# Optimization experiments

Measured on AMD Instinct MI355X. Metric: run time of the kernel, lower is better.

The kernel has to match this reference:

```python
import jax, jax.numpy as jnp
import numpy as np

D = 196; NCH = 64; H = 8; DH = 64; INNER = H * DH; MLP = 784; SEQ = 65


def _ln(x, g, b, eps=1e-5):
    m = x.mean(-1, keepdims=True)
    v = x.var(-1, keepdims=True)
    return (x - m) / jnp.sqrt(v + eps) * g + b


def setup_inputs() -> dict:
    key = jax.random.key(0)
    ks = jax.random.split(key, 12)
    f = jax.random.normal
    return dict(
        x=f(ks[0], (1, SEQ, D), dtype=jnp.float32),
        tokens=f(ks[1], (1, D), dtype=jnp.float32),
        x_pe=f(ks[2], (1, NCH, D), dtype=jnp.float32),
        conv_k=f(ks[3], (3, 3), dtype=jnp.float32) * 0.3,   # Conv2d(1,1,3) kernel
        bn_g=jnp.ones(()), bn_b=jnp.zeros(()), bn_rm=jnp.zeros(()), bn_rv=jnp.ones(()),
        fc_w1=f(ks[4], (NCH, 12)) * 0.1,
        fc_w2=f(ks[5], (12, NCH)) * 0.1,
        ln1_g=jnp.ones((D,)), ln1_b=jnp.zeros((D,)),
        ln2_g=jnp.ones((D,)), ln2_b=jnp.zeros((D,)),
        w_qkv=f(ks[6], (D, 3 * INNER)) * 0.05,
        w_out=f(ks[7], (INNER, D)) * 0.05, b_out=jnp.zeros((D,)),
        ff_w1=f(ks[8], (D, MLP)) * 0.05, ff_b1=jnp.zeros((MLP,)),
        ff_w2=f(ks[9], (MLP, D)) * 0.05, ff_b2=jnp.zeros((D,)),
    )


def reference(x, tokens, x_pe, conv_k, bn_g, bn_b, bn_rm, bn_rv,
              fc_w1, fc_w2, ln1_g, ln1_b, ln2_g, ln2_b,
              w_qkv, w_out, b_out, ff_w1, ff_b1, ff_w2, ff_b2):
    # --- per-channel Conv2d(1,1,3,p=1)+BN+ReLU, batched over all 64 rows ---
    # Each row is (1,1,1,196): height 1 with pad 1 means the top/bottom kernel
    # rows only touch zero padding, so only the middle kernel row contributes
    # -> equivalent to a 1D conv with kernel conv_k[1].
    rows = x_pe[0]                      # [64,196]
    km = conv_k[1]                      # [3]
    xp = jnp.pad(rows, ((0, 0), (1, 1)))
    conv = km[0] * xp[:, :D] + km[1] * xp[:, 1:D + 1] + km[2] * xp[:, 2:D + 2]
    bn = (conv - bn_rm) / jnp.sqrt(bn_rv + 1e-5) * bn_g + bn_b
    a = jax.nn.relu(bn)                 # [64,196]  (== x_AfterConv / a)

    # --- sort-based suppress/excitation channel gating ---
    b1 = a.mean(-1)                     # [64] adaptive avg pool
    val = jnp.sort(b1)
    idx = jnp.argsort(b1)
    middle = jnp.where((val.max() < 0) | (val.min() > 0),
                       jnp.int32(32), jnp.argmax(val > 0).astype(jnp.int32))
    rank = jnp.argsort(idx)             # rank of each channel in ascending order
    sup = rank < middle                 # channels in idx[:middle]
    l_s = middle.astype(b1.dtype)
    l_e = (NCH - middle).astype(b1.dtype)
    b2 = jnp.where(sup,
                   b1 - 1.0 / (1.0 + jnp.power(l_s, b1)),
                   b1 + 1.0 / (1.0 + jnp.power(l_e, -b1)))

    c = jax.nn.sigmoid(jax.nn.relu(b2 @ fc_w1) @ fc_w2)   # [64]
    x_att = a * c[:, None]                                  # [64,196]
    x_att = jnp.concatenate([x_att, tokens.reshape(1, D)], axis=0)[None]  # [1,65,196]

    # --- PreNorm attention ---
    h = _ln(x, ln1_g, ln1_b)
    qkv = h @ w_qkv
    q, k, v = jnp.split(qkv, 3, axis=-1)
    def heads(t):
        return t.reshape(1, SEQ, H, DH).transpose(0, 2, 1, 3)  # b h n d
    q, k, v = heads(q), heads(k), heads(v)
    attn = jax.nn.softmax(jnp.einsum('bhnd,bhmd->bhnm', q, k) * (DH ** -0.5), axis=-1)
    o = jnp.einsum('bhnm,bhmd->bhnd', attn, v).transpose(0, 2, 1, 3).reshape(1, SEQ, INNER)
    x = o @ w_out + b_out + x + x_att

    # --- PreNorm feed-forward ---
    h2 = _ln(x, ln2_g, ln2_b)
    x = (jax.nn.gelu(h2 @ ff_w1 + ff_b1, approximate=False) @ ff_w2 + ff_b2) + x
    return x
```

## Files before the change

kernel.cpp:

```cpp
#include <hip/hip_runtime.h>
#include <math.h>

#define D 196
#define NCH 64
#define NH 8
#define DHD 64
#define INNER 512
#define MLP 784
#define SEQ 65

__device__ __forceinline__ float bsum(float v, float* red) {
    for (int off = 32; off > 0; off >>= 1) v += __shfl_down(v, off, 64);
    int lane = threadIdx.x & 63, wid = threadIdx.x >> 6;
    if (lane == 0) red[wid] = v;
    __syncthreads();
    float s = red[0] + red[1] + red[2] + red[3];
    __syncthreads();
    return s;
}

__device__ __forceinline__ float bsum8(float v, float* red) {
    for (int off = 32; off > 0; off >>= 1) v += __shfl_down(v, off, 64);
    int lane = threadIdx.x & 63, wid = threadIdx.x >> 6;
    if (lane == 0) red[wid] = v;
    __syncthreads();
    float s = red[0] + red[1] + red[2] + red[3] + red[4] + red[5] + red[6] + red[7];
    __syncthreads();
    return s;
}

__global__ void __launch_bounds__(256) k1(const float* __restrict__ x_pe,
        const float* __restrict__ conv_k, const float* __restrict__ bn_g,
        const float* __restrict__ bn_b, const float* __restrict__ bn_rm,
        const float* __restrict__ bn_rv, const float* __restrict__ x,
        const float* __restrict__ ln1_g, const float* __restrict__ ln1_b,
        const float* __restrict__ w_qkv,
        float* __restrict__ a, float* __restrict__ b1, float* __restrict__ qkv) {
    __shared__ float red[4];
    __shared__ float h[D];
    __shared__ float ps[512];
    int b = blockIdx.x, t = threadIdx.x;
    if (b < NCH) {
        const float* row = x_pe + b * D;
        float val = 0.f;
        if (t < D) {
            float km0 = conv_k[3], km1 = conv_k[4], km2 = conv_k[5];
            float inv = rsqrtf(bn_rv[0] + 1e-5f);
            float l = (t > 0) ? row[t - 1] : 0.f;
            float m = row[t];
            float r = (t < D - 1) ? row[t + 1] : 0.f;
            float conv = km0 * l + km1 * m + km2 * r;
            float bn = (conv - bn_rm[0]) * inv * bn_g[0] + bn_b[0];
            val = fmaxf(bn, 0.f);
            a[b * D + t] = val;
        }
        float tot = bsum(val, red);
        if (t == 0) b1[b] = tot * (1.f / (float)D);
    } else {
        int qb = b - NCH;
        int n = qb / 12, cg = qb % 12;
        const float* row = x + n * D;
        float v = (t < D) ? row[t] : 0.f;
        float mean = bsum(v, red) * (1.f / (float)D);
        float d = (t < D) ? (v - mean) : 0.f;
        float var = bsum(d * d, red) * (1.f / (float)D);
        float rinv = rsqrtf(var + 1e-5f);
        if (t < D) h[t] = d * rinv * ln1_g[t] + ln1_b[t];
        __syncthreads();
        int qq = t >> 6, lt = t & 63;
        int c0 = cg * 128 + lt * 2;
        const float* wp = w_qkv + (qq * 49) * 1536 + c0;
        const float* hp = h + qq * 49;
        float a0 = 0.f, a1 = 0.f;
#pragma unroll
        for (int i = 0; i < 49; i++) {
            float2 w2 = *(const float2*)(wp + i * 1536);
            float hv = hp[i];
            a0 += hv * w2.x;
            a1 += hv * w2.y;
        }
        ps[qq * 128 + lt * 2] = a0;
        ps[qq * 128 + lt * 2 + 1] = a1;
        __syncthreads();
        if (t < 64) {
            float s0 = ps[t * 2] + ps[128 + t * 2] + ps[256 + t * 2] + ps[384 + t * 2];
            float s1 = ps[t * 2 + 1] + ps[129 + t * 2] + ps[257 + t * 2] + ps[385 + t * 2];
            float2 o2 = make_float2(s0, s1);
            *(float2*)(qkv + n * 1536 + cg * 128 + t * 2) = o2;
        }
    }
}

__global__ void __launch_bounds__(512) k2(const float* __restrict__ b1,
        const float* __restrict__ fc_w1, const float* __restrict__ fc_w2,
        const float* __restrict__ qkv, const float* __restrict__ w_out,
        const float* __restrict__ b_out, const float* __restrict__ x,
        const float* __restrict__ a, const float* __restrict__ tokens,
        const float* __restrict__ ln2_g, const float* __restrict__ ln2_b,
        const float* __restrict__ ff_b2,
        float* __restrict__ h2g, float* __restrict__ out) {
    __shared__ float red[8];
    __shared__ float sq[512];
    __shared__ float pp[8 * 80];
    __shared__ float so[512];
    __shared__ float ps[784];
    __shared__ float x2row[D];
    __shared__ float sb1[NCH];
    __shared__ float sb2[NCH];
    __shared__ float hid[12];
    __shared__ float cgate;

    int n = blockIdx.x, t = threadIdx.x;

    sq[t] = qkv[n * 1536 + t];
    if (t < NCH) sb1[t] = b1[t];
    __syncthreads();
    if (t < NCH) {
        float v = sb1[t];
        float mx = -1e30f, mn = 1e30f;
        int cle = 0, rank = 0;
        for (int j = 0; j < NCH; j++) {
            float w = sb1[j];
            mx = fmaxf(mx, w);
            mn = fminf(mn, w);
            if (w <= 0.f) cle++;
            if (w < v || (w == v && j < t)) rank++;
        }
        int middle;
        if (mx < 0.f || mn > 0.f) middle = 32;
        else if (mx <= 0.f) middle = 0;
        else middle = cle;
        float b2;
        if (rank < middle) {
            float ls = (float)middle;
            b2 = v - 1.f / (1.f + powf(ls, v));
        } else {
            float le = (float)(NCH - middle);
            b2 = v + 1.f / (1.f + powf(le, -v));
        }
        sb2[t] = b2;
    }
    __syncthreads();
    if (t < 12) {
        float s = 0.f;
        for (int j = 0; j < NCH; j++) s += sb2[j] * fc_w1[j * 12 + t];
        hid[t] = fmaxf(s, 0.f);
    }
    __syncthreads();
    if (t == 0 && n < NCH) {
        float s = 0.f;
        for (int k = 0; k < 12; k++) s += hid[k] * fc_w2[k * NCH + n];
        cgate = 1.f / (1.f + expf(-s));
    }
    __syncthreads();

    const float scale = 0.125f;
    int w = t >> 6, L = t & 63;
    const float4* kr = (const float4*)(qkv + L * 1536 + INNER + w * DHD);
    const float4* q4 = (const float4*)(sq + w * DHD);
    float s = 0.f;
#pragma unroll
    for (int i = 0; i < 16; i++) {
        float4 kv = kr[i];
        float4 qv = q4[i];
        s += qv.x * kv.x + qv.y * kv.y + qv.z * kv.z + qv.w * kv.w;
    }
    float sL = s * scale;
    float t64 = sq[w * DHD + L] * qkv[64 * 1536 + INNER + w * DHD + L];
#pragma unroll
    for (int off = 1; off < 64; off <<= 1) t64 += __shfl_xor(t64, off, 64);
    float s64 = t64 * scale;
    float mx = sL;
#pragma unroll
    for (int off = 1; off < 64; off <<= 1) mx = fmaxf(mx, __shfl_xor(mx, off, 64));
    mx = fmaxf(mx, s64);
    float e = expf(sL - mx);
    float e64 = expf(s64 - mx);
    float esum = e;
#pragma unroll
    for (int off = 1; off < 64; off <<= 1) esum += __shfl_xor(esum, off, 64);
    esum += e64;
    float rs = 1.f / esum;
    pp[w * 80 + L] = e;
    if (L == 0) pp[w * 80 + 64] = e64;
    __syncthreads();
    float acc = 0.f;
#pragma unroll 13
    for (int m = 0; m < SEQ; m++)
        acc += pp[w * 80 + m] * qkv[m * 1536 + 2 * INNER + w * DHD + L];
    so[w * DHD + L] = acc * rs;
    __syncthreads();

    if (t < 392) {
        int qq = t / 98, p = t - qq * 98;
        const float* wp = w_out + (qq * 128) * D + 2 * p;
        const float* op = so + qq * 128;
        float a0 = 0.f, a1 = 0.f;
#pragma unroll 16
        for (int i = 0; i < 128; i++) {
            float2 w2 = *(const float2*)(wp + i * D);
            float ov = op[i];
            a0 += ov * w2.x;
            a1 += ov * w2.y;
        }
        ps[qq * 196 + 2 * p] = a0;
        ps[qq * 196 + 2 * p + 1] = a1;
    }
    __syncthreads();
    if (t < 98) {
        float s0 = ps[2 * t] + ps[196 + 2 * t] + ps[392 + 2 * t] + ps[588 + 2 * t];
        float s1 = ps[2 * t + 1] + ps[197 + 2 * t] + ps[393 + 2 * t] + ps[589 + 2 * t];
        float2 xr = *(const float2*)(x + n * D + 2 * t);
        float2 br = *(const float2*)(b_out + 2 * t);
        x2row[2 * t] = s0 + xr.x + br.x;
        x2row[2 * t + 1] = s1 + xr.y + br.y;
    }
    __syncthreads();

    if (t < D) {
        float att = (n < NCH) ? a[n * D + t] * cgate : tokens[t];
        float xv = x2row[t] + att;
        x2row[t] = xv;
        out[n * D + t] = xv + ff_b2[t];
    }
    __syncthreads();

    float v = (t < D) ? x2row[t] : 0.f;
    float mean = bsum8(v, red) * (1.f / (float)D);
    float d = (t < D) ? (v - mean) : 0.f;
    float var = bsum8(d * d, red) * (1.f / (float)D);
    float rinv = rsqrtf(var + 1e-5f);
    if (t < D) h2g[n * D + t] = d * rinv * ln2_g[t] + ln2_b[t];
}

__global__ void __launch_bounds__(256) k3(const float* __restrict__ h2g,
        const float* __restrict__ ff_w1, const float* __restrict__ ff_b1,
        const float* __restrict__ ff_w2, float* __restrict__ out) {
    __shared__ float h2s[D];
    __shared__ float st[98];
    __shared__ float ps[392];
    int n = blockIdx.x, cg = blockIdx.y, t = threadIdx.x;
    if (t < D) h2s[t] = h2g[n * D + t];
    __syncthreads();
    if (t < D) {
        int qq = t / 49, p = t - qq * 49;
        int c0 = cg * 98 + 2 * p;
        const float* wp = ff_w1 + (qq * 49) * MLP + c0;
        const float* hp = h2s + qq * 49;
        float a0 = 0.f, a1 = 0.f;
#pragma unroll
        for (int i = 0; i < 49; i++) {
            float2 w2 = *(const float2*)(wp + i * MLP);
            float hv = hp[i];
            a0 += hv * w2.x;
            a1 += hv * w2.y;
        }
        if (qq == 0) { a0 += ff_b1[c0]; a1 += ff_b1[c0 + 1]; }
        ps[qq * 98 + 2 * p] = a0;
        ps[qq * 98 + 2 * p + 1] = a1;
    }
    __syncthreads();
    if (t < 49) {
        float s0 = ps[2 * t] + ps[98 + 2 * t] + ps[196 + 2 * t] + ps[294 + 2 * t];
        float s1 = ps[2 * t + 1] + ps[99 + 2 * t] + ps[197 + 2 * t] + ps[295 + 2 * t];
        st[2 * t] = 0.5f * s0 * (1.f + erff(s0 * 0.70710678118f));
        st[2 * t + 1] = 0.5f * s1 * (1.f + erff(s1 * 0.70710678118f));
    }
    __syncthreads();
    if (t < D) {
        int hh = t / 98, p = t - hh * 98;
        const float* wp = ff_w2 + (cg * 98 + hh * 49) * D + 2 * p;
        const float* sp = st + hh * 49;
        float a0 = 0.f, a1 = 0.f;
#pragma unroll
        for (int i = 0; i < 49; i++) {
            float2 w2 = *(const float2*)(wp + i * D);
            float sv = sp[i];
            a0 += sv * w2.x;
            a1 += sv * w2.y;
        }
        ps[hh * 196 + 2 * p] = a0;
        ps[hh * 196 + 2 * p + 1] = a1;
    }
    __syncthreads();
    if (t < 98) {
        float s0 = ps[2 * t] + ps[196 + 2 * t];
        float s1 = ps[2 * t + 1] + ps[197 + 2 * t];
        atomicAdd(&out[n * D + 2 * t], s0);
        atomicAdd(&out[n * D + 2 * t + 1], s1);
    }
}

extern "C" void kernel_launch(void* const* d_in, const int* in_sizes, int n_in,
                              void* d_out, int out_size, void* d_ws, size_t ws_size,
                              hipStream_t stream) {
    const float* x      = (const float*)d_in[0];
    const float* tokens = (const float*)d_in[1];
    const float* x_pe   = (const float*)d_in[2];
    const float* conv_k = (const float*)d_in[3];
    const float* bn_g   = (const float*)d_in[4];
    const float* bn_b   = (const float*)d_in[5];
    const float* bn_rm  = (const float*)d_in[6];
    const float* bn_rv  = (const float*)d_in[7];
    const float* fc_w1  = (const float*)d_in[8];
    const float* fc_w2  = (const float*)d_in[9];
    const float* ln1_g  = (const float*)d_in[10];
    const float* ln1_b  = (const float*)d_in[11];
    const float* ln2_g  = (const float*)d_in[12];
    const float* ln2_b  = (const float*)d_in[13];
    const float* w_qkv  = (const float*)d_in[14];
    const float* w_out  = (const float*)d_in[15];
    const float* b_out  = (const float*)d_in[16];
    const float* ff_w1  = (const float*)d_in[17];
    const float* ff_b1  = (const float*)d_in[18];
    const float* ff_w2  = (const float*)d_in[19];
    const float* ff_b2  = (const float*)d_in[20];
    float* out = (float*)d_out;

    float* ws = (float*)d_ws;
    float* a    = ws;
    float* b1   = ws + 12544;
    float* qkv  = ws + 12608;
    float* h2g  = ws + 112448;

    k1<<<844, 256, 0, stream>>>(x_pe, conv_k, bn_g, bn_b, bn_rm, bn_rv,
                                x, ln1_g, ln1_b, w_qkv, a, b1, qkv);
    k2<<<SEQ, 512, 0, stream>>>(b1, fc_w1, fc_w2, qkv, w_out, b_out, x,
                                a, tokens, ln2_g, ln2_b, ff_b2, h2g, out);
    k3<<<dim3(SEQ, 8), 256, 0, stream>>>(h2g, ff_w1, ff_b1, ff_w2, out);
}
```

Before: 137.4 us.

## Split attention kernel across head groups and move LayerNorm2 into FFN kernel

The attention/output-projection kernel now runs two 256-thread blocks per token, each handling four heads. Partial output-projection results are combined with atomics into a workspace row that k1 zeroes beforehand. LayerNorm2 and the residual/bias add move into the feed-forward kernel, and each of its column-group blocks recomputes the row norm. This raises parallelism in the latency-bound middle stage and drops the h2g round trip. The costs are redundant LN work in k3, extra atomics, and reliance on single-wavefront ordering for some shared-memory reads that no longer have a barrier.

```diff
diff --git a/kernel.cpp b/kernel.cpp
--- a/kernel.cpp
+++ b/kernel.cpp
@@ -19,28 +19,21 @@
     return s;
 }
 
-__device__ __forceinline__ float bsum8(float v, float* red) {
-    for (int off = 32; off > 0; off >>= 1) v += __shfl_down(v, off, 64);
-    int lane = threadIdx.x & 63, wid = threadIdx.x >> 6;
-    if (lane == 0) red[wid] = v;
-    __syncthreads();
-    float s = red[0] + red[1] + red[2] + red[3] + red[4] + red[5] + red[6] + red[7];
-    __syncthreads();
-    return s;
-}
-
 __global__ void __launch_bounds__(256) k1(const float* __restrict__ x_pe,
         const float* __restrict__ conv_k, const float* __restrict__ bn_g,
         const float* __restrict__ bn_b, const float* __restrict__ bn_rm,
         const float* __restrict__ bn_rv, const float* __restrict__ x,
         const float* __restrict__ ln1_g, const float* __restrict__ ln1_b,
         const float* __restrict__ w_qkv,
-        float* __restrict__ a, float* __restrict__ b1, float* __restrict__ qkv) {
+        float* __restrict__ a, float* __restrict__ b1, float* __restrict__ qkv,
+        float* __restrict__ out, float* __restrict__ x2g) {
     __shared__ float red[4];
     __shared__ float h[D];
     __shared__ float ps[512];
     int b = blockIdx.x, t = threadIdx.x;
     if (b < NCH) {
+        int zi = b * 200 + t;
+        if (t < 200 && zi < SEQ * D) { out[zi] = 0.f; x2g[zi] = 0.f; }
         const float* row = x_pe + b * D;
         float val = 0.f;
         if (t < D) {
@@ -91,72 +84,67 @@
     }
 }
 
-__global__ void __launch_bounds__(512) k2(const float* __restrict__ b1,
+__global__ void __launch_bounds__(256) k2(const float* __restrict__ b1,
         const float* __restrict__ fc_w1, const float* __restrict__ fc_w2,
         const float* __restrict__ qkv, const float* __restrict__ w_out,
         const float* __restrict__ b_out, const float* __restrict__ x,
         const float* __restrict__ a, const float* __restrict__ tokens,
-        const float* __restrict__ ln2_g, const float* __restrict__ ln2_b,
-        const float* __restrict__ ff_b2,
-        float* __restrict__ h2g, float* __restrict__ out) {
-    __shared__ float red[8];
-    __shared__ float sq[512];
-    __shared__ float pp[8 * 80];
-    __shared__ float so[512];
+        float* __restrict__ x2g) {
+    __shared__ float sq[256];
+    __shared__ float pp[4 * 80];
+    __shared__ float so[256];
     __shared__ float ps[784];
-    __shared__ float x2row[D];
     __shared__ float sb1[NCH];
     __shared__ float sb2[NCH];
     __shared__ float hid[12];
     __shared__ float cgate;
 
-    int n = blockIdx.x, t = threadIdx.x;
-
-    sq[t] = qkv[n * 1536 + t];
-    if (t < NCH) sb1[t] = b1[t];
-    __syncthreads();
-    if (t < NCH) {
-        float v = sb1[t];
-        float mx = -1e30f, mn = 1e30f;
-        int cle = 0, rank = 0;
-        for (int j = 0; j < NCH; j++) {
-            float w = sb1[j];
-            mx = fmaxf(mx, w);
-            mn = fminf(mn, w);
-            if (w <= 0.f) cle++;
-            if (w < v || (w == v && j < t)) rank++;
-        }
-        int middle;
-        if (mx < 0.f || mn > 0.f) middle = 32;
-        else if (mx <= 0.f) middle = 0;
-        else middle = cle;
-        float b2;
-        if (rank < middle) {
-            float ls = (float)middle;
-            b2 = v - 1.f / (1.f + powf(ls, v));
-        } else {
-            float le = (float)(NCH - middle);
-            b2 = v + 1.f / (1.f + powf(le, -v));
-        }
-        sb2[t] = b2;
-    }
-    __syncthreads();
-    if (t < 12) {
-        float s = 0.f;
-        for (int j = 0; j < NCH; j++) s += sb2[j] * fc_w1[j * 12 + t];
-        hid[t] = fmaxf(s, 0.f);
-    }
-    __syncthreads();
-    if (t == 0 && n < NCH) {
-        float s = 0.f;
-        for (int k = 0; k < 12; k++) s += hid[k] * fc_w2[k * NCH + n];
-        cgate = 1.f / (1.f + expf(-s));
-    }
-    __syncthreads();
+    int n = blockIdx.x, g = blockIdx.y, t = threadIdx.x;
+    int w = t >> 6, L = t & 63, head = g * 4 + w;
+
+    sq[t] = qkv[n * 1536 + g * 256 + t];
+
+    if (g == 0) {
+        if (t < NCH) {
+            sb1[t] = b1[t];
+            float v = b1[t];
+            float mx = -1e30f, mn = 1e30f;
+            int cle = 0, rank = 0;
+            for (int j = 0; j < NCH; j++) {
+                float ww = sb1[j];
+                mx = fmaxf(mx, ww);
+                mn = fminf(mn, ww);
+                if (ww <= 0.f) cle++;
+                if (ww < v || (ww == v && j < t)) rank++;
+            }
+            int middle;
+            if (mx < 0.f || mn > 0.f) middle = 32;
+            else if (mx <= 0.f) middle = 0;
+            else middle = cle;
+            float b2;
+            if (rank < middle) {
+                float ls = (float)middle;
+                b2 = v - 1.f / (1.f + powf(ls, v));
+            } else {
+                float le = (float)(NCH - middle);
+                b2 = v + 1.f / (1.f + powf(le, -v));
+            }
+            sb2[t] = b2;
+        }
+        if (t < 12) {
+            float s = 0.f;
+            for (int j = 0; j < NCH; j++) s += sb2[j] * fc_w1[j * 12 + t];
+            hid[t] = fmaxf(s, 0.f);
+        }
+        if (t == 0 && n < NCH) {
+            float s = 0.f;
+            for (int k = 0; k < 12; k++) s += hid[k] * fc_w2[k * NCH + n];
+            cgate = 1.f / (1.f + expf(-s));
+        }
+    }
 
     const float scale = 0.125f;
-    int w = t >> 6, L = t & 63;
-    const float4* kr = (const float4*)(qkv + L * 1536 + INNER + w * DHD);
+    const float4* kr = (const float4*)(qkv + L * 1536 + INNER + head * DHD);
     const float4* q4 = (const float4*)(sq + w * DHD);
     float s = 0.f;
 #pragma unroll
@@ -166,7 +154,7 @@
         s += qv.x * kv.x + qv.y * kv.y + qv.z * kv.z + qv.w * kv.w;
     }
     float sL = s * scale;
-    float t64 = sq[w * DHD + L] * qkv[64 * 1536 + INNER + w * DHD + L];
+    float t64 = sq[w * DHD + L] * qkv[64 * 1536 + INNER + head * DHD + L];
 #pragma unroll
     for (int off = 1; off < 64; off <<= 1) t64 += __shfl_xor(t64, off, 64);
     float s64 = t64 * scale;
@@ -183,64 +171,61 @@
     float rs = 1.f / esum;
     pp[w * 80 + L] = e;
     if (L == 0) pp[w * 80 + 64] = e64;
-    __syncthreads();
     float acc = 0.f;
 #pragma unroll 13
     for (int m = 0; m < SEQ; m++)
-        acc += pp[w * 80 + m] * qkv[m * 1536 + 2 * INNER + w * DHD + L];
+        acc += pp[w * 80 + m] * qkv[m * 1536 + 2 * INNER + head * DHD + L];
     so[w * DHD + L] = acc * rs;
     __syncthreads();
 
-    if (t < 392) {
-        int qq = t / 98, p = t - qq * 98;
-        const float* wp = w_out + (qq * 128) * D + 2 * p;
-        const float* op = so + qq * 128;
-        float a0 = 0.f, a1 = 0.f;
+    if (t < 196) {
+        int qq = t / 49, quad = t - qq * 49;
+        const float* wp = w_out + (g * 256 + qq * 64) * D + 4 * quad;
+        const float* op = so + qq * 64;
+        float a0 = 0.f, a1 = 0.f, a2 = 0.f, a3 = 0.f;
 #pragma unroll 16
-        for (int i = 0; i < 128; i++) {
-            float2 w2 = *(const float2*)(wp + i * D);
+        for (int i = 0; i < 64; i++) {
+            float4 w4 = *(const float4*)(wp + i * D);
             float ov = op[i];
-            a0 += ov * w2.x;
-            a1 += ov * w2.y;
-        }
-        ps[qq * 196 + 2 * p] = a0;
-        ps[qq * 196 + 2 * p + 1] = a1;
-    }
-    __syncthreads();
-    if (t < 98) {
-        float s0 = ps[2 * t] + ps[196 + 2 * t] + ps[392 + 2 * t] + ps[588 + 2 * t];
-        float s1 = ps[2 * t + 1] + ps[197 + 2 * t] + ps[393 + 2 * t] + ps[589 + 2 * t];
-        float2 xr = *(const float2*)(x + n * D + 2 * t);
-        float2 br = *(const float2*)(b_out + 2 * t);
-        x2row[2 * t] = s0 + xr.x + br.x;
-        x2row[2 * t + 1] = s1 + xr.y + br.y;
-    }
-    __syncthreads();
-
-    if (t < D) {
-        float att = (n < NCH) ? a[n * D + t] * cgate : tokens[t];
-        float xv = x2row[t] + att;
-        x2row[t] = xv;
-        out[n * D + t] = xv + ff_b2[t];
-    }
-    __syncthreads();
-
-    float v = (t < D) ? x2row[t] : 0.f;
-    float mean = bsum8(v, red) * (1.f / (float)D);
-    float d = (t < D) ? (v - mean) : 0.f;
-    float var = bsum8(d * d, red) * (1.f / (float)D);
-    float rinv = rsqrtf(var + 1e-5f);
-    if (t < D) h2g[n * D + t] = d * rinv * ln2_g[t] + ln2_b[t];
-}
-
-__global__ void __launch_bounds__(256) k3(const float* __restrict__ h2g,
+            a0 += ov * w4.x;
+            a1 += ov * w4.y;
+            a2 += ov * w4.z;
+            a3 += ov * w4.w;
+        }
+        ps[qq * 196 + 4 * quad]     = a0;
+        ps[qq * 196 + 4 * quad + 1] = a1;
+        ps[qq * 196 + 4 * quad + 2] = a2;
+        ps[qq * 196 + 4 * quad + 3] = a3;
+    }
+    __syncthreads();
+    if (t < 196) {
+        float sacc = ps[t] + ps[196 + t] + ps[392 + t] + ps[588 + t];
+        if (g == 0) {
+            float att = (n < NCH) ? a[n * D + t] * cgate : tokens[t];
+            sacc += x[n * D + t] + b_out[t] + att;
+        }
+        atomicAdd(&x2g[n * D + t], sacc);
+    }
+}
+
+__global__ void __launch_bounds__(256) k3(const float* __restrict__ x2g,
+        const float* __restrict__ ln2_g, const float* __restrict__ ln2_b,
         const float* __restrict__ ff_w1, const float* __restrict__ ff_b1,
-        const float* __restrict__ ff_w2, float* __restrict__ out) {
+        const float* __restrict__ ff_w2, const float* __restrict__ ff_b2,
+        float* __restrict__ out) {
+    __shared__ float red[4];
+    __shared__ float x2s[D];
     __shared__ float h2s[D];
     __shared__ float st[98];
     __shared__ float ps[392];
     int n = blockIdx.x, cg = blockIdx.y, t = threadIdx.x;
-    if (t < D) h2s[t] = h2g[n * D + t];
+    float v = 0.f;
+    if (t < D) { v = x2g[n * D + t]; x2s[t] = v; }
+    float mean = bsum(v, red) * (1.f / (float)D);
+    float d = (t < D) ? (v - mean) : 0.f;
+    float var = bsum(d * d, red) * (1.f / (float)D);
+    float rinv = rsqrtf(var + 1e-5f);
+    if (t < D) h2s[t] = d * rinv * ln2_g[t] + ln2_b[t];
     __syncthreads();
     if (t < D) {
         int qq = t / 49, p = t - qq * 49;
@@ -286,6 +271,10 @@
     if (t < 98) {
         float s0 = ps[2 * t] + ps[196 + 2 * t];
         float s1 = ps[2 * t + 1] + ps[197 + 2 * t];
+        if (cg == 0) {
+            s0 += ff_b2[2 * t] + x2s[2 * t];
+            s1 += ff_b2[2 * t + 1] + x2s[2 * t + 1];
+        }
         atomicAdd(&out[n * D + 2 * t], s0);
         atomicAdd(&out[n * D + 2 * t + 1], s1);
     }
@@ -321,11 +310,12 @@
     float* a    = ws;
     float* b1   = ws + 12544;
     float* qkv  = ws + 12608;
-    float* h2g  = ws + 112448;
+    float* x2g  = ws + 112448;
 
     k1<<<844, 256, 0, stream>>>(x_pe, conv_k, bn_g, bn_b, bn_rm, bn_rv,
-                                x, ln1_g, ln1_b, w_qkv, a, b1, qkv);
-    k2<<<SEQ, 512, 0, stream>>>(b1, fc_w1, fc_w2, qkv, w_out, b_out, x,
-                                a, tokens, ln2_g, ln2_b, ff_b2, h2g, out);
-    k3<<<dim3(SEQ, 8), 256, 0, stream>>>(h2g, ff_w1, ff_b1, ff_w2, out);
-}
+                                x, ln1_g, ln1_b, w_qkv, a, b1, qkv, out, x2g);
+    k2<<<dim3(SEQ, 2), 256, 0, stream>>>(b1, fc_w1, fc_w2, qkv, w_out, b_out,
+                                         x, a, tokens, x2g);
+    k3<<<dim3(SEQ, 8), 256, 0, stream>>>(x2g, ln2_g, ln2_b,
+                                         ff_w1, ff_b1, ff_w2, ff_b2, out);
+}
```

Result: faster. 130.6 us (-5.0%).
